# Optimization experiments

Hardware: AMD Instinct MI355X
Metric: run time of the kernel (lower is better)

## Reference

```python
import jax, jax.numpy as jnp
import numpy as np
from jax import lax

E = 192      # hidden size
NH = 6       # attention heads
L = 6        # mixer blocks (permutation length)
CO = 256     # merging output channels
KH, KW = 7, 11   # locality window
LOCAL = (False, False, True, True, True, True)
B, H, W = 64, 8, 64


def skew(x, pad_value):
    # shift every row one step right, turning columns into diagonals (torch skew)
    rest = x.shape[:-2]
    Hd, Wd = x.shape[-2], x.shape[-1]
    x = jnp.pad(x, [(0, 0)] * (x.ndim - 1) + [(0, Hd)], constant_values=pad_value)
    x = x.reshape(*rest, -1)[..., : Hd * (Hd + Wd - 1)]
    x = x.reshape(*rest, Hd, Hd + Wd - 1)
    end = (Hd + Wd - 1) - (Wd // 2) + (Wd % 2 - 1)
    return x[..., Wd // 2 : end]


def make_mask(h, w, kh, kw):
    # boolean [h*w, h*w]; True inside the local window (torch: True = NOT allowed)
    m = jnp.ones((h, w, kh, kw), dtype=bool)
    m = m.transpose(0, 2, 1, 3)        # [h, kh, w, kw]
    m = skew(m, 0)                     # [h, kh, w, w]
    m = m.transpose(2, 3, 0, 1)        # [w, w, h, kh]
    m = skew(m, 0)                     # [w, w, h, h]
    m = m.transpose(2, 0, 3, 1)        # [h, w, h, w]
    return m.reshape(h * w, h * w)


def layernorm(x, g, b, eps=1e-5):
    mu = jnp.mean(x, axis=-1, keepdims=True)
    var = jnp.mean((x - mu) ** 2, axis=-1, keepdims=True)
    return (x - mu) / jnp.sqrt(var + eps) * g + b


def mha(x, mask, wi, bi, wo, bo, nh):
    # torch nn.MultiheadAttention (batch_first, self-attn, inference)
    b, s, e = x.shape
    hd = e // nh
    qkv = x @ wi.T + bi                                   # [b, s, 3e]
    q, k, v = jnp.split(qkv, 3, axis=-1)
    to_heads = lambda t: t.reshape(b, s, nh, hd).transpose(0, 2, 1, 3)
    q, k, v = to_heads(q), to_heads(k), to_heads(v)
    scores = jnp.einsum('bhqd,bhkd->bhqk', q, k) / jnp.sqrt(jnp.asarray(hd, x.dtype))
    if mask is not None:
        scores = jnp.where(mask, -jnp.inf, scores)
    attn = jax.nn.softmax(scores, axis=-1)
    out = jnp.einsum('bhqk,bhkd->bhqd', attn, v)
    out = out.transpose(0, 2, 1, 3).reshape(b, s, e)
    return out @ wo.T + bo


def mixer_block(x, mask, wi, bi, wo, bo, g1, b1, g2, b2, wm1, bm1, wm2, bm2):
    x = layernorm(x, g1, b1)
    x = mha(x, mask, wi, bi, wo, bo, NH) + x
    x = layernorm(x, g2, b2)
    h = jax.nn.relu(x @ wm1.T + bm1)
    return h @ wm2.T + bm2 + x


def fvtr_stage(image, in_w, in_b, out_w, out_b, ln1_g, ln1_b, ln2_g, ln2_b,
               w1, b1, w2, b2, conv_w, conv_b, mln_g, mln_b):
    bsz, c, h, w = image.shape
    x = jnp.swapaxes(image, -1, -3).reshape(bsz, w * h, c)   # [B, W*H, C]
    mask = make_mask(h, w, KH, KW)
    for i, loc in enumerate(LOCAL):
        x = mixer_block(x, mask if loc else None,
                        in_w[i], in_b[i], out_w[i], out_b[i],
                        ln1_g[i], ln1_b[i], ln2_g[i], ln2_b[i],
                        w1[i], b1[i], w2[i], b2[i])
    x = jnp.swapaxes(x.reshape(bsz, w, h, c), -1, -3)        # [B, C, H, W]
    # MergingBlock: conv (3,1) stride (2,1) pad (1,0) + channel LayerNorm
    y = lax.conv_general_dilated(x, conv_w, window_strides=(2, 1),
                                 padding=((1, 1), (0, 0)),
                                 dimension_numbers=('NCHW', 'OIHW', 'NCHW'))
    y = y + conv_b[None, :, None, None]
    y = jnp.moveaxis(y, 1, -1)
    y = layernorm(y, mln_g, mln_b)
    return jnp.moveaxis(y, -1, 1)


def setup_inputs() -> dict:
    key = jax.random.key(0)
    ks = jax.random.split(key, 8)
    s = 0.02
    return {
        'image': jax.random.normal(ks[0], (B, E, H, W), jnp.float32),
        'in_w':  s * jax.random.normal(ks[1], (L, 3 * E, E), jnp.float32),
        'in_b':  jnp.zeros((L, 3 * E), jnp.float32),
        'out_w': s * jax.random.normal(ks[2], (L, E, E), jnp.float32),
        'out_b': jnp.zeros((L, E), jnp.float32),
        'ln1_g': jnp.ones((L, E), jnp.float32),
        'ln1_b': jnp.zeros((L, E), jnp.float32),
        'ln2_g': jnp.ones((L, E), jnp.float32),
        'ln2_b': jnp.zeros((L, E), jnp.float32),
        'w1':    s * jax.random.normal(ks[3], (L, 4 * E, E), jnp.float32),
        'b1':    jnp.zeros((L, 4 * E), jnp.float32),
        'w2':    s * jax.random.normal(ks[4], (L, E, 4 * E), jnp.float32),
        'b2':    jnp.zeros((L, E), jnp.float32),
        'conv_w': s * jax.random.normal(ks[5], (CO, E, 3, 1), jnp.float32),
        'conv_b': jnp.zeros((CO,), jnp.float32),
        'mln_g': jnp.ones((CO,), jnp.float32),
        'mln_b': jnp.zeros((CO,), jnp.float32),
    }


def reference(image, in_w, in_b, out_w, out_b, ln1_g, ln1_b, ln2_g, ln2_b,
              w1, b1, w2, b2, conv_w, conv_b, mln_g, mln_b):
    return fvtr_stage(image, in_w, in_b, out_w, out_b, ln1_g, ln1_b, ln2_g, ln2_b,
                      w1, b1, w2, b2, conv_w, conv_b, mln_g, mln_b)
```

## Files before the change

kernel.cpp:

```cpp
#include <hip/hip_runtime.h>
#include <hip/hip_bf16.h>
#include <math.h>

#define Bn   64
#define Ssz  512
#define Ed   192
#define NHd  6
#define HDd  32
#define Ld   6
#define COd  256
#define Himg 8
#define Wimg 64
#define Mrows (Bn*Ssz)

typedef unsigned int  uint;
typedef unsigned short ushort;
using short8 = __attribute__((ext_vector_type(8))) short;
using f32x4  = __attribute__((ext_vector_type(4))) float;

__device__ inline ushort f2b(float f) {
    uint u = __builtin_bit_cast(uint, f);
    u = (u + 0x7FFFu + ((u >> 16) & 1u)) >> 16;
    return (ushort)u;
}

__device__ __forceinline__ float fexp2(float x) {
#if __has_builtin(__builtin_amdgcn_exp2f)
    return __builtin_amdgcn_exp2f(x);
#else
    return exp2f(x);
#endif
}

__device__ __forceinline__ uint cvt_pk_bf16(float a, float b) {
    uint r;
    asm("v_cvt_pk_bf16_f32 %0, %1, %2" : "=v"(r) : "v"(a), "v"(b));
    return r;
}

__device__ __forceinline__ void gload16(const ushort* g, ushort* l, int lane) {
#if __has_builtin(__builtin_amdgcn_global_load_lds)
    __builtin_amdgcn_global_load_lds(
        (const __attribute__((address_space(1))) uint*)g,
        (__attribute__((address_space(3))) uint*)l, 16, 0, 0);
#else
    *(uint4*)(l + (size_t)lane * 8) = *(const uint4*)g;
#endif
}

__global__ __launch_bounds__(256) void reshape_in(const float* __restrict__ img,
                                                  float* __restrict__ X) {
    int t = blockIdx.x * 256 + threadIdx.x;
    int c = t % Ed;
    int s = (t / Ed) % Ssz;
    int b = t / (Ed * Ssz);
    int w = s >> 3, h = s & 7;
    X[t] = img[(((size_t)b * Ed + c) * Himg + h) * Wimg + w];
}

__global__ __launch_bounds__(256) void f2b_arr(const float* __restrict__ in,
                                               ushort* __restrict__ out, int n) {
    int t = blockIdx.x * 256 + threadIdx.x;
    if (t < n) out[t] = f2b(in[t]);
}

__global__ __launch_bounds__(256) void conv_w_to_bf16(const float* __restrict__ cw,
                                                      ushort* __restrict__ out) {
    int t = blockIdx.x * 256 + threadIdx.x;
    if (t >= COd * 576) return;
    int co = t / 576, rem = t % 576;
    int kh = rem / Ed, c = rem % Ed;
    out[t] = f2b(cw[((size_t)co * Ed + c) * 3 + kh]);
}

__global__ __launch_bounds__(256) void ln_kernel(const float* __restrict__ in,
                                                 float* __restrict__ out,
                                                 ushort* __restrict__ outb,
                                                 const float* __restrict__ g,
                                                 const float* __restrict__ bb) {
    int row  = blockIdx.x * 4 + (threadIdx.x >> 6);
    int lane = threadIdx.x & 63;
    bool act = lane < 48;
    float4 v = make_float4(0.f, 0.f, 0.f, 0.f);
    if (act) v = ((const float4*)(in + (size_t)row * Ed))[lane];
    float s = v.x + v.y + v.z + v.w;
    #pragma unroll
    for (int off = 32; off > 0; off >>= 1) s += __shfl_xor(s, off);
    float mu = s * (1.f / 192.f);
    float4 d = make_float4(v.x - mu, v.y - mu, v.z - mu, v.w - mu);
    float qv = act ? (d.x*d.x + d.y*d.y + d.z*d.z + d.w*d.w) : 0.f;
    #pragma unroll
    for (int off = 32; off > 0; off >>= 1) qv += __shfl_xor(qv, off);
    float rstd = rsqrtf(qv * (1.f / 192.f) + 1e-5f);
    if (act) {
        float4 gg  = ((const float4*)g)[lane];
        float4 bbv = ((const float4*)bb)[lane];
        float4 y = make_float4(d.x * rstd * gg.x + bbv.x,
                               d.y * rstd * gg.y + bbv.y,
                               d.z * rstd * gg.z + bbv.z,
                               d.w * rstd * gg.w + bbv.w);
        ((float4*)(out + (size_t)row * Ed))[lane] = y;
        ushort4 yb;
        yb.x = f2b(y.x); yb.y = f2b(y.y); yb.z = f2b(y.z); yb.w = f2b(y.w);
        *(ushort4*)(outb + (size_t)row * Ed + lane * 4) = yb;
    }
}

template<int RELU, int RESID, int OBF, int VOUT>
__global__ __launch_bounds__(256) void gemm_mfma(
    const ushort* __restrict__ A, const ushort* __restrict__ Wt,
    const float* __restrict__ bias, const float* __restrict__ resid,
    float* __restrict__ C, ushort* __restrict__ Cb,
    ushort* __restrict__ qpout, ushort* __restrict__ kpout,
    ushort* __restrict__ vtout,
    int M, int N, int K)
{
    __shared__ __align__(16) ushort As[12288];
    __shared__ __align__(16) ushort Bs[6144];
    const int tid  = threadIdx.x;
    const int lane = tid & 63;
    const int wave = tid >> 6;
    const int wr = wave >> 1, wc = wave & 1;
    const int bm = blockIdx.x * 128;
    const int bn = blockIdx.y * 64;

    const ushort* Ag[6]; ushort* Al[6];
    #pragma unroll
    for (int i = 0; i < 6; ++i) {
        int fa = 4 * i + wave;
        int msub = fa / 3, ksub = fa % 3;
        int m = msub * 16 + (lane & 15);
        int k = ksub * 32 + ((lane >> 4) << 3);
        Ag[i] = A + (size_t)(bm + m) * K + k;
        Al[i] = As + fa * 512;
    }
    const ushort* Bg[3]; ushort* Bl[3];
    #pragma unroll
    for (int i = 0; i < 3; ++i) {
        int fb = 4 * i + wave;
        int nsub = fb / 3, ksub = fb % 3;
        int n = nsub * 16 + (lane & 15);
        int k = ksub * 32 + ((lane >> 4) << 3);
        Bg[i] = Wt + (size_t)(bn + n) * K + k;
        Bl[i] = Bs + fb * 512;
    }

    f32x4 acc[4][2];
    #pragma unroll
    for (int i = 0; i < 4; ++i)
        #pragma unroll
        for (int j = 0; j < 2; ++j) acc[i][j] = (f32x4){0.f, 0.f, 0.f, 0.f};

    for (int k0 = 0; k0 < K; k0 += 96) {
        #pragma unroll
        for (int i = 0; i < 6; ++i) gload16(Ag[i] + k0, Al[i], lane);
        #pragma unroll
        for (int i = 0; i < 3; ++i) gload16(Bg[i] + k0, Bl[i], lane);
        __syncthreads();
        #pragma unroll
        for (int ksub = 0; ksub < 3; ++ksub) {
            short8 af[4], bf[2];
            #pragma unroll
            for (int ms = 0; ms < 4; ++ms)
                af[ms] = *(const short8*)(As + (((wr*4+ms)*3 + ksub) * 64 + lane) * 8);
            #pragma unroll
            for (int ns = 0; ns < 2; ++ns)
                bf[ns] = *(const short8*)(Bs + (((wc*2+ns)*3 + ksub) * 64 + lane) * 8);
            #pragma unroll
            for (int ms = 0; ms < 4; ++ms)
                #pragma unroll
                for (int ns = 0; ns < 2; ++ns)
                    acc[ms][ns] = __builtin_amdgcn_mfma_f32_16x16x32_bf16(
                        af[ms], bf[ns], acc[ms][ns], 0, 0, 0);
        }
        __syncthreads();
    }

    int q = lane >> 4, colL = lane & 15;
    #pragma unroll
    for (int ms = 0; ms < 4; ++ms) {
        #pragma unroll
        for (int ns = 0; ns < 2; ++ns) {
            int row0 = bm + (wr*4 + ms) * 16 + q * 4;
            int col  = bn + (wc*2 + ns) * 16 + colL;
            float bvv = bias[col];
            float v[4];
            #pragma unroll
            for (int r = 0; r < 4; ++r) {
                v[r] = acc[ms][ns][r] + bvv;
                if (RELU) v[r] = fmaxf(v[r], 0.f);
                if (RESID) v[r] += resid[(size_t)(row0 + r) * N + col];
            }
            if (VOUT) {
                int bidx = row0 >> 9, srow = row0 & 511;
                if (col >= 384) {
                    int hh = (col - 384) >> 5, dd = (col - 384) & 31;
                    int sr = srow ^ ((((srow >> 2) ^ (srow >> 3)) & 1) * 12);
                    ushort4 pv;
                    pv.x = f2b(v[0]); pv.y = f2b(v[1]); pv.z = f2b(v[2]); pv.w = f2b(v[3]);
                    *(ushort4*)(vtout + (((size_t)(bidx * NHd + hh) * 32 + dd) << 9) + sr) = pv;
                } else {
                    ushort* dst = (col < 192) ? qpout : kpout;
                    int cc = (col < 192) ? col : col - 192;
                    if (col < 192) {
                        const float c2 = 0.2550547270628364f;
                        #pragma unroll
                        for (int r = 0; r < 4; ++r) v[r] *= c2;
                    }
                    int hh = cc >> 5, dd = cc & 31;
                    ushort* p = dst + ((size_t)(bidx * NHd + hh) << 14) + (size_t)srow * 32 + dd;
                    p[0]  = f2b(v[0]); p[32] = f2b(v[1]);
                    p[64] = f2b(v[2]); p[96] = f2b(v[3]);
                }
            } else {
                #pragma unroll
                for (int r = 0; r < 4; ++r) {
                    if (OBF) Cb[(size_t)(row0 + r) * N + col] = f2b(v[r]);
                    else     C [(size_t)(row0 + r) * N + col] = v[r];
                }
            }
        }
    }
}

template<int KIT, int LNOUT>
__global__ __launch_bounds__(256) void gemm_ln(
    const ushort* __restrict__ A, const ushort* __restrict__ Wt,
    const float* __restrict__ bias, const float* __restrict__ resid,
    const float* __restrict__ lng, const float* __restrict__ lnb,
    float* __restrict__ outf, ushort* __restrict__ outb)
{
    __shared__ __align__(16) ushort As[4096];
    __shared__ __align__(16) ushort Bs[12288];
    const int K = KIT * 64;
    const int lane = threadIdx.x & 63;
    const int wave = threadIdx.x >> 6;
    const int g = lane >> 4, ql = lane & 15;
    const int bm = blockIdx.x * 64;

    const ushort* Gp[8]; ushort* Lp[8];
    #pragma unroll
    for (int i = 0; i < 8; ++i) {
        int f = 4 * i + wave;
        if (f < 8) {
            int msub = f >> 1, ksub = f & 1;
            Gp[i] = A + (size_t)(bm + msub * 16 + ql) * K + ksub * 32 + g * 8;
            Lp[i] = As + f * 512;
        } else {
            int fb = f - 8, nsub = fb >> 1, ksub = fb & 1;
            Gp[i] = Wt + (size_t)(nsub * 16 + ql) * K + ksub * 32 + g * 8;
            Lp[i] = Bs + fb * 512;
        }
    }

    f32x4 acc[12];
    #pragma unroll
    for (int i = 0; i < 12; ++i) acc[i] = (f32x4){0.f, 0.f, 0.f, 0.f};

    for (int kc = 0; kc < KIT; ++kc) {
        #pragma unroll
        for (int i = 0; i < 8; ++i) gload16(Gp[i] + kc * 64, Lp[i], lane);
        __syncthreads();
        #pragma unroll
        for (int ksub = 0; ksub < 2; ++ksub) {
            short8 af = *(const short8*)(As + ((wave * 2 + ksub) * 64 + lane) * 8);
            #pragma unroll
            for (int ns = 0; ns < 12; ++ns) {
                short8 bf = *(const short8*)(Bs + ((ns * 2 + ksub) * 64 + lane) * 8);
                acc[ns] = __builtin_amdgcn_mfma_f32_16x16x32_bf16(af, bf, acc[ns], 0, 0, 0);
            }
        }
        __syncthreads();
    }

    float bi[12], gg[12], bb[12];
    #pragma unroll
    for (int ns = 0; ns < 12; ++ns) {
        int col = ns * 16 + ql;
        bi[ns] = bias[col];
        if (LNOUT) { gg[ns] = lng[col]; bb[ns] = lnb[col]; }
    }
    #pragma unroll
    for (int r = 0; r < 4; ++r) {
        int row = bm + wave * 16 + g * 4 + r;
        float v[12];
        #pragma unroll
        for (int ns = 0; ns < 12; ++ns)
            v[ns] = acc[ns][r] + bi[ns] + resid[(size_t)row * Ed + ns * 16 + ql];
        if (LNOUT) {
            float s = 0.f;
            #pragma unroll
            for (int ns = 0; ns < 12; ++ns) s += v[ns];
            s += __shfl_xor(s, 1); s += __shfl_xor(s, 2);
            s += __shfl_xor(s, 4); s += __shfl_xor(s, 8);
            float mu = s * (1.f / 192.f);
            float qv = 0.f;
            #pragma unroll
            for (int ns = 0; ns < 12; ++ns) { float d = v[ns] - mu; qv += d * d; }
            qv += __shfl_xor(qv, 1); qv += __shfl_xor(qv, 2);
            qv += __shfl_xor(qv, 4); qv += __shfl_xor(qv, 8);
            float rstd = rsqrtf(qv * (1.f / 192.f) + 1e-5f);
            #pragma unroll
            for (int ns = 0; ns < 12; ++ns) {
                float y = (v[ns] - mu) * rstd * gg[ns] + bb[ns];
                int col = ns * 16 + ql;
                outf[(size_t)row * Ed + col] = y;
                outb[(size_t)row * Ed + col] = f2b(y);
            }
        } else {
            #pragma unroll
            for (int ns = 0; ns < 12; ++ns)
                outf[(size_t)row * Ed + ns * 16 + ql] = v[ns];
        }
    }
}

template<int USE_MASK>
__global__ __launch_bounds__(256) void attn_mfma(const ushort* __restrict__ qp,
                                                 const ushort* __restrict__ kp,
                                                 const ushort* __restrict__ vt,
                                                 ushort* __restrict__ att) {
    const int bh = blockIdx.x;
    const int b = bh / NHd, h = bh % NHd;
    const int wave = threadIdx.x >> 6, lane = threadIdx.x & 63;
    const int g = lane >> 4, ql = lane & 15;
    const int qb = blockIdx.y * 128 + wave * 32;

    const ushort* qbase = qp + ((size_t)bh << 14);
    const ushort* kbase = kp + ((size_t)bh << 14);
    const ushort* vbase = vt + ((size_t)bh << 14);
    short8 qf[2];
    #pragma unroll
    for (int t = 0; t < 2; ++t)
        qf[t] = *(const short8*)(qbase + (size_t)(qb + t * 16 + ql) * 32 + g * 8);

    short8 onesf;
    #pragma unroll
    for (int j = 0; j < 8; ++j) onesf[j] = (short)0x3F80;

    uint m0[2], m1[2]; int qh[2];
    if (USE_MASK) {
        #pragma unroll
        for (int t = 0; t < 2; ++t) {
            int qwt = ((qb + t * 16) & 63) + ql;
            qh[t] = (qb + t * 16) >> 6;
            uint a0 = 0, a1 = 0;
            #pragma unroll
            for (int i = 0; i < 8; ++i) {
                int keyl = (i >> 2) * 16 + 4 * g + (i & 3);
                int d0 = keyl - qwt;      d0 = d0 < 0 ? -d0 : d0;
                int d1 = keyl + 32 - qwt; d1 = d1 < 0 ? -d1 : d1;
                if (d0 <= 5) a0 |= (1u << i);
                if (d1 <= 5) a1 |= (1u << i);
            }
            m0[t] = a0; m1[t] = a1;
        }
    }

    f32x4 o0[2], o1[2], o2[2];
    #pragma unroll
    for (int t = 0; t < 2; ++t) {
        o0[t] = (f32x4){0.f,0.f,0.f,0.f};
        o1[t] = (f32x4){0.f,0.f,0.f,0.f};
        o2[t] = (f32x4){0.f,0.f,0.f,0.f};
    }
    const f32x4 z = {0.f,0.f,0.f,0.f};

    short8 kb_[3][2];
    short8 vb_[2][2];
    f32x4  st_[2][4];
    short8 pa[2];

    auto LK = [&](int kt, short8* d) {
        d[0] = *(const short8*)(kbase + (size_t)(kt * 32 + ql) * 32 + g * 8);
        d[1] = *(const short8*)(kbase + (size_t)(kt * 32 + 16 + ql) * 32 + g * 8);
    };
    auto LV = [&](int kt, short8* d) {
        d[0] = *(const short8*)(vbase + (size_t)ql * 512 + kt * 32 + 8 * g);
        d[1] = *(const short8*)(vbase + (size_t)(16 + ql) * 512 + kt * 32 + 8 * g);
    };
    auto S = [&](const short8* k, f32x4* st) {
        st[0] = __builtin_amdgcn_mfma_f32_16x16x32_bf16(k[0], qf[0], z, 0, 0, 0);
        st[1] = __builtin_amdgcn_mfma_f32_16x16x32_bf16(k[1], qf[0], z, 0, 0, 0);
        st[2] = __builtin_amdgcn_mfma_f32_16x16x32_bf16(k[0], qf[1], z, 0, 0, 0);
        st[3] = __builtin_amdgcn_mfma_f32_16x16x32_bf16(k[1], qf[1], z, 0, 0, 0);
    };
    auto F = [&](int kt, const f32x4* st) {
        #pragma unroll
        for (int t = 0; t < 2; ++t) {
            float p8[8];
            #pragma unroll
            for (int r = 0; r < 4; ++r) {
                p8[r]     = fexp2(st[t*2][r]);
                p8[4 + r] = fexp2(st[t*2+1][r]);
            }
            if (USE_MASK) {
                int dh = (kt >> 1) - qh[t]; dh = dh < 0 ? -dh : dh;
                if (dh <= 3) {
                    uint mm = (kt & 1) ? m1[t] : m0[t];
                    #pragma unroll
                    for (int i = 0; i < 8; ++i)
                        if ((mm >> i) & 1u) p8[i] = 0.f;
                }
            }
            uint Au = cvt_pk_bf16(p8[0], p8[1]);
            uint Bu = cvt_pk_bf16(p8[2], p8[3]);
            uint Cu = cvt_pk_bf16(p8[4], p8[5]);
            uint Du = cvt_pk_bf16(p8[6], p8[7]);
            asm("v_permlane32_swap_b32 %0, %1" : "+v"(Au), "+v"(Cu));
            asm("v_permlane32_swap_b32 %0, %1" : "+v"(Bu), "+v"(Du));
            union { uint u[4]; short8 s; } pk;
            pk.u[0] = Au; pk.u[1] = Bu; pk.u[2] = Cu; pk.u[3] = Du;
            pa[t] = pk.s;
        }
    };
    auto PV = [&](const short8* v) {
        #pragma unroll
        for (int t = 0; t < 2; ++t) {
            o0[t] = __builtin_amdgcn_mfma_f32_16x16x32_bf16(pa[t], v[0], o0[t], 0, 0, 0);
            o1[t] = __builtin_amdgcn_mfma_f32_16x16x32_bf16(pa[t], v[1], o1[t], 0, 0, 0);
            o2[t] = __builtin_amdgcn_mfma_f32_16x16x32_bf16(pa[t], onesf, o2[t], 0, 0, 0);
        }
    };

    LK(0, kb_[0]); LK(1, kb_[1]); LK(2, kb_[2]);
    LV(0, vb_[0]); LV(1, vb_[1]);
    S(kb_[0], st_[0]);
    #pragma unroll
    for (int kt = 0; kt < 16; ++kt) {
        if (kt < 15) S(kb_[(kt + 1) % 3], st_[(kt + 1) & 1]);
        if (kt < 13) LK(kt + 3, kb_[kt % 3]);
        F(kt, st_[kt & 1]);
        __builtin_amdgcn_s_setprio(1);
        PV(vb_[kt & 1]);
        __builtin_amdgcn_s_setprio(0);
        if (kt < 14) LV(kt + 2, vb_[kt & 1]);
    }

    ushort* op = att + (size_t)b * Ssz * Ed + h * 32;
    #pragma unroll
    for (int t = 0; t < 2; ++t) {
        #pragma unroll
        for (int r = 0; r < 4; ++r) {
            float iv = 1.f / o2[t][r];
            int row = qb + t * 16 + 4 * g + r;
            op[(size_t)row * Ed + ql]      = f2b(o0[t][r] * iv);
            op[(size_t)row * Ed + 16 + ql] = f2b(o1[t][r] * iv);
        }
    }
}

__global__ __launch_bounds__(256) void im2col(const float* __restrict__ X,
                                              ushort* __restrict__ A2) {
    int t = blockIdx.x * 256 + threadIdx.x;
    int col = t % 576;
    int r   = t / 576;
    int kh = col / Ed, c = col % Ed;
    int w = r & 63, ho = (r >> 6) & 3, b = r >> 8;
    int hin = 2 * ho + kh - 1;
    float v = 0.f;
    if (hin >= 0 && hin < Himg)
        v = X[((size_t)(b * Ssz + w * Himg + hin)) * Ed + c];
    A2[t] = f2b(v);
}

__global__ __launch_bounds__(256) void ln_out_kernel(const float* __restrict__ C2,
                                                     const float* __restrict__ g,
                                                     const float* __restrict__ beta,
                                                     float* __restrict__ out) {
    __shared__ float lds[32 * 257];
    int w0 = blockIdx.x * 32, ho = blockIdx.y, b = blockIdx.z;
    int tid = threadIdx.x;
    size_t rbase = ((size_t)b * 4 + ho) * 64 + w0;

    for (int i = 0; i < 32; ++i)
        lds[i * 257 + tid] = C2[(rbase + i) * COd + tid];
    __syncthreads();

    int wv = tid >> 6, lane = tid & 63;
    for (int rr = 0; rr < 8; ++rr) {
        int i = wv * 8 + rr;
        float v0 = lds[i*257 + lane], v1 = lds[i*257 + lane + 64];
        float v2 = lds[i*257 + lane + 128], v3 = lds[i*257 + lane + 192];
        float s = v0 + v1 + v2 + v3;
        #pragma unroll
        for (int off = 32; off > 0; off >>= 1) s += __shfl_xor(s, off);
        float mu = s * (1.f / 256.f);
        float d0 = v0-mu, d1 = v1-mu, d2 = v2-mu, d3 = v3-mu;
        float qv = d0*d0 + d1*d1 + d2*d2 + d3*d3;
        #pragma unroll
        for (int off = 32; off > 0; off >>= 1) qv += __shfl_xor(qv, off);
        float rstd = rsqrtf(qv * (1.f / 256.f) + 1e-5f);
        lds[i*257 + lane]       = d0 * rstd * g[lane]       + beta[lane];
        lds[i*257 + lane + 64]  = d1 * rstd * g[lane + 64]  + beta[lane + 64];
        lds[i*257 + lane + 128] = d2 * rstd * g[lane + 128] + beta[lane + 128];
        lds[i*257 + lane + 192] = d3 * rstd * g[lane + 192] + beta[lane + 192];
    }
    __syncthreads();

    int w = tid & 31, half = tid >> 5;
    for (int j = 0; j < 32; ++j) {
        int co = half + j * 8;
        out[(((size_t)b * COd + co) * 4 + ho) * Wimg + w0 + w] = lds[w * 257 + co];
    }
}

extern "C" void kernel_launch(void* const* d_in, const int* in_sizes, int n_in,
                              void* d_out, int out_size, void* d_ws, size_t ws_size,
                              hipStream_t stream) {
    const float* image = (const float*)d_in[0];
    const float* in_w  = (const float*)d_in[1];
    const float* in_b  = (const float*)d_in[2];
    const float* out_w = (const float*)d_in[3];
    const float* out_b = (const float*)d_in[4];
    const float* ln1_g = (const float*)d_in[5];
    const float* ln1_b = (const float*)d_in[6];
    const float* ln2_g = (const float*)d_in[7];
    const float* ln2_b = (const float*)d_in[8];
    const float* w1    = (const float*)d_in[9];
    const float* b1    = (const float*)d_in[10];
    const float* w2    = (const float*)d_in[11];
    const float* b2    = (const float*)d_in[12];
    const float* convw = (const float*)d_in[13];
    const float* convb = (const float*)d_in[14];
    const float* mln_g = (const float*)d_in[15];
    const float* mln_b = (const float*)d_in[16];
    float* out = (float*)d_out;
    float* ws  = (float*)d_ws;

    float* F1   = ws;
    float* F2   = ws + 6291456;
    float* BIG  = ws + 12582912;
    ushort* QP   = (ushort*)BIG;
    ushort* KP   = (ushort*)(BIG + 3145728);
    ushort* VT   = (ushort*)(BIG + 6291456);
    ushort* Hb   = (ushort*)BIG;
    ushort* A2b  = (ushort*)BIG;
    float*  C2   = BIG + 4718592;
    ushort* XNb  = (ushort*)(BIG + 12582912);
    ushort* ATTb = (ushort*)(ws + 28311552);
    ushort* Wb   = (ushort*)(ws + 31457280);

    ushort* in_wb  = Wb;
    ushort* out_wb = Wb + 663552;
    ushort* w1b    = Wb + 884736;
    ushort* w2b    = Wb + 1769472;
    ushort* cwb    = Wb + 2654208;

    reshape_in<<<Mrows * Ed / 256, 256, 0, stream>>>(image, F2);
    f2b_arr<<<(663552 + 255) / 256, 256, 0, stream>>>(in_w,  in_wb,  663552);
    f2b_arr<<<(221184 + 255) / 256, 256, 0, stream>>>(out_w, out_wb, 221184);
    f2b_arr<<<(884736 + 255) / 256, 256, 0, stream>>>(w1,    w1b,    884736);
    f2b_arr<<<(884736 + 255) / 256, 256, 0, stream>>>(w2,    w2b,    884736);
    conv_w_to_bf16<<<(147456 + 255) / 256, 256, 0, stream>>>(convw, cwb);

    ln_kernel<<<Mrows / 4, 256, 0, stream>>>(F2, F1, XNb, ln1_g, ln1_b);

    for (int i = 0; i < Ld; ++i) {
        gemm_mfma<0,0,1,1><<<dim3(Mrows/128, 9), 256, 0, stream>>>(
            XNb, in_wb + (size_t)i * 3*Ed*Ed, in_b + i * 3*Ed,
            nullptr, nullptr, nullptr, QP, KP, VT, Mrows, 3*Ed, Ed);
        if (i >= 2) attn_mfma<1><<<dim3(Bn * NHd, 4), 256, 0, stream>>>(QP, KP, VT, ATTb);
        else        attn_mfma<0><<<dim3(Bn * NHd, 4), 256, 0, stream>>>(QP, KP, VT, ATTb);
        gemm_ln<3,1><<<Mrows/64, 256, 0, stream>>>(
            ATTb, out_wb + (size_t)i * Ed*Ed, out_b + i*Ed,
            F1, ln2_g + i*Ed, ln2_b + i*Ed, F2, XNb);
        gemm_mfma<1,0,1,0><<<dim3(Mrows/128, 12), 256, 0, stream>>>(
            XNb, w1b + (size_t)i * 4*Ed*Ed, b1 + i * 4*Ed,
            nullptr, nullptr, Hb, nullptr, nullptr, nullptr, Mrows, 4*Ed, Ed);
        if (i < Ld - 1) {
            gemm_ln<12,1><<<Mrows/64, 256, 0, stream>>>(
                Hb, w2b + (size_t)i * 4*Ed*Ed, b2 + i*Ed,
                F2, ln1_g + (i+1)*Ed, ln1_b + (i+1)*Ed, F1, XNb);
        } else {
            gemm_ln<12,0><<<Mrows/64, 256, 0, stream>>>(
                Hb, w2b + (size_t)i * 4*Ed*Ed, b2 + i*Ed,
                F2, nullptr, nullptr, F1, nullptr);
        }
    }

    im2col<<<9437184 / 256, 256, 0, stream>>>(F1, A2b);
    gemm_mfma<0,0,0,0><<<dim3(16384/128, 4), 256, 0, stream>>>(
        A2b, cwb, convb, nullptr, C2, nullptr, nullptr, nullptr, nullptr,
        16384, COd, 576);
    ln_out_kernel<<<dim3(2, 4, Bn), 256, 0, stream>>>(C2, mln_g, mln_b, out);
}
```

Before: 1.081 ms.

## Fuse im2col into final MLP GEMM epilogue and merge weight conversions

```diff
diff --git a/kernel.cpp b/kernel.cpp
--- a/kernel.cpp
+++ b/kernel.cpp
@@ -58,19 +58,26 @@
     X[t] = img[(((size_t)b * Ed + c) * Himg + h) * Wimg + w];
 }
 
-__global__ __launch_bounds__(256) void f2b_arr(const float* __restrict__ in,
-                                               ushort* __restrict__ out, int n) {
+__global__ __launch_bounds__(256) void cvt_weights(const float* __restrict__ in_w,
+                                                   const float* __restrict__ out_w,
+                                                   const float* __restrict__ w1,
+                                                   const float* __restrict__ w2,
+                                                   const float* __restrict__ convw,
+                                                   ushort* __restrict__ Wb) {
     int t = blockIdx.x * 256 + threadIdx.x;
-    if (t < n) out[t] = f2b(in[t]);
-}
-
-__global__ __launch_bounds__(256) void conv_w_to_bf16(const float* __restrict__ cw,
-                                                      ushort* __restrict__ out) {
-    int t = blockIdx.x * 256 + threadIdx.x;
-    if (t >= COd * 576) return;
-    int co = t / 576, rem = t % 576;
-    int kh = rem / Ed, c = rem % Ed;
-    out[t] = f2b(cw[((size_t)co * Ed + c) * 3 + kh]);
+    if (t >= 2801664) return;
+    float v;
+    if (t < 663552)        v = in_w[t];
+    else if (t < 884736)   v = out_w[t - 663552];
+    else if (t < 1769472)  v = w1[t - 884736];
+    else if (t < 2654208)  v = w2[t - 1769472];
+    else {
+        int u = t - 2654208;
+        int co = u / 576, rem = u % 576;
+        int kh = rem / Ed, c = rem % Ed;
+        v = convw[((size_t)co * Ed + c) * 3 + kh];
+    }
+    Wb[t] = f2b(v);
 }
 
 __global__ __launch_bounds__(256) void ln_kernel(const float* __restrict__ in,
@@ -223,12 +230,13 @@
     }
 }
 
-template<int KIT, int LNOUT>
+template<int KIT, int MODE>
 __global__ __launch_bounds__(256) void gemm_ln(
     const ushort* __restrict__ A, const ushort* __restrict__ Wt,
     const float* __restrict__ bias, const float* __restrict__ resid,
     const float* __restrict__ lng, const float* __restrict__ lnb,
-    float* __restrict__ outf, ushort* __restrict__ outb)
+    float* __restrict__ outf, ushort* __restrict__ outb,
+    ushort* __restrict__ a2out)
 {
     __shared__ __align__(16) ushort As[4096];
     __shared__ __align__(16) ushort Bs[12288];
@@ -278,7 +286,7 @@
     for (int ns = 0; ns < 12; ++ns) {
         int col = ns * 16 + ql;
         bi[ns] = bias[col];
-        if (LNOUT) { gg[ns] = lng[col]; bb[ns] = lnb[col]; }
+        if (MODE == 1) { gg[ns] = lng[col]; bb[ns] = lnb[col]; }
     }
     #pragma unroll
     for (int r = 0; r < 4; ++r) {
@@ -287,7 +295,7 @@
         #pragma unroll
         for (int ns = 0; ns < 12; ++ns)
             v[ns] = acc[ns][r] + bi[ns] + resid[(size_t)row * Ed + ns * 16 + ql];
-        if (LNOUT) {
+        if (MODE == 1) {
             float s = 0.f;
             #pragma unroll
             for (int ns = 0; ns < 12; ++ns) s += v[ns];
@@ -306,6 +314,25 @@
                 int col = ns * 16 + ql;
                 outf[(size_t)row * Ed + col] = y;
                 outb[(size_t)row * Ed + col] = f2b(y);
+            }
+        } else if (MODE == 2) {
+            int bz = row >> 9, s = row & 511;
+            int w = s >> 3, h = s & 7;
+            #pragma unroll
+            for (int ho = 0; ho < 4; ++ho) {
+                int kh = h + 1 - 2 * ho;
+                if (kh >= 0 && kh < 3) {
+                    size_t r2 = ((size_t)((bz * 4 + ho) * 64 + w)) * 576 + kh * 192;
+                    #pragma unroll
+                    for (int ns = 0; ns < 12; ++ns)
+                        a2out[r2 + ns * 16 + ql] = f2b(v[ns]);
+                }
+            }
+            if (h == 0) {
+                size_t r2 = ((size_t)(bz * 4 * 64 + w)) * 576;
+                #pragma unroll
+                for (int ns = 0; ns < 12; ++ns)
+                    a2out[r2 + ns * 16 + ql] = 0;
             }
         } else {
             #pragma unroll
@@ -448,20 +475,6 @@
             op[(size_t)row * Ed + 16 + ql] = f2b(o1[t][r] * iv);
         }
     }
-}
-
-__global__ __launch_bounds__(256) void im2col(const float* __restrict__ X,
-                                              ushort* __restrict__ A2) {
-    int t = blockIdx.x * 256 + threadIdx.x;
-    int col = t % 576;
-    int r   = t / 576;
-    int kh = col / Ed, c = col % Ed;
-    int w = r & 63, ho = (r >> 6) & 3, b = r >> 8;
-    int hin = 2 * ho + kh - 1;
-    float v = 0.f;
-    if (hin >= 0 && hin < Himg)
-        v = X[((size_t)(b * Ssz + w * Himg + hin)) * Ed + c];
-    A2[t] = f2b(v);
 }
 
 __global__ __launch_bounds__(256) void ln_out_kernel(const float* __restrict__ C2,
@@ -535,9 +548,9 @@
     ushort* KP   = (ushort*)(BIG + 3145728);
     ushort* VT   = (ushort*)(BIG + 6291456);
     ushort* Hb   = (ushort*)BIG;
-    ushort* A2b  = (ushort*)BIG;
     float*  C2   = BIG + 4718592;
     ushort* XNb  = (ushort*)(BIG + 12582912);
+    ushort* A2b  = (ushort*)(ws + 25165824);
     ushort* ATTb = (ushort*)(ws + 28311552);
     ushort* Wb   = (ushort*)(ws + 31457280);
 
@@ -548,11 +561,8 @@
     ushort* cwb    = Wb + 2654208;
 
     reshape_in<<<Mrows * Ed / 256, 256, 0, stream>>>(image, F2);
-    f2b_arr<<<(663552 + 255) / 256, 256, 0, stream>>>(in_w,  in_wb,  663552);
-    f2b_arr<<<(221184 + 255) / 256, 256, 0, stream>>>(out_w, out_wb, 221184);
-    f2b_arr<<<(884736 + 255) / 256, 256, 0, stream>>>(w1,    w1b,    884736);
-    f2b_arr<<<(884736 + 255) / 256, 256, 0, stream>>>(w2,    w2b,    884736);
-    conv_w_to_bf16<<<(147456 + 255) / 256, 256, 0, stream>>>(convw, cwb);
+    cvt_weights<<<(2801664 + 255) / 256, 256, 0, stream>>>(
+        in_w, out_w, w1, w2, convw, Wb);
 
     ln_kernel<<<Mrows / 4, 256, 0, stream>>>(F2, F1, XNb, ln1_g, ln1_b);
 
@@ -564,22 +574,21 @@
         else        attn_mfma<0><<<dim3(Bn * NHd, 4), 256, 0, stream>>>(QP, KP, VT, ATTb);
         gemm_ln<3,1><<<Mrows/64, 256, 0, stream>>>(
             ATTb, out_wb + (size_t)i * Ed*Ed, out_b + i*Ed,
-            F1, ln2_g + i*Ed, ln2_b + i*Ed, F2, XNb);
+            F1, ln2_g + i*Ed, ln2_b + i*Ed, F2, XNb, nullptr);
         gemm_mfma<1,0,1,0><<<dim3(Mrows/128, 12), 256, 0, stream>>>(
             XNb, w1b + (size_t)i * 4*Ed*Ed, b1 + i * 4*Ed,
             nullptr, nullptr, Hb, nullptr, nullptr, nullptr, Mrows, 4*Ed, Ed);
         if (i < Ld - 1) {
             gemm_ln<12,1><<<Mrows/64, 256, 0, stream>>>(
                 Hb, w2b + (size_t)i * 4*Ed*Ed, b2 + i*Ed,
-                F2, ln1_g + (i+1)*Ed, ln1_b + (i+1)*Ed, F1, XNb);
+                F2, ln1_g + (i+1)*Ed, ln1_b + (i+1)*Ed, F1, XNb, nullptr);
         } else {
-            gemm_ln<12,0><<<Mrows/64, 256, 0, stream>>>(
+            gemm_ln<12,2><<<Mrows/64, 256, 0, stream>>>(
                 Hb, w2b + (size_t)i * 4*Ed*Ed, b2 + i*Ed,
-                F2, nullptr, nullptr, F1, nullptr);
-        }
-    }
-
-    im2col<<<9437184 / 256, 256, 0, stream>>>(F1, A2b);
+                F2, nullptr, nullptr, nullptr, nullptr, A2b);
+        }
+    }
+
     gemm_mfma<0,0,0,0><<<dim3(16384/128, 4), 256, 0, stream>>>(
         A2b, cwb, convb, nullptr, C2, nullptr, nullptr, nullptr, nullptr,
         16384, COd, 576);
```

After: 1.059 ms. 2.1% less time.
